# Performance work log

Measured on AMD Instinct MI355X. Metric: run time of the kernel, lower is better.

## Reference

```python
import jax, jax.numpy as jnp
import numpy as np

WS = 8      # window size
NH = 8      # num heads
ED = 256    # embed dim
HD = ED // NH  # head dim


def conv2d(x, w, b):
    # x: [B,C,H,W], w: [O,I,3,3] (torch OIHW), SAME padding, stride 1
    y = jax.lax.conv_general_dilated(x, w, (1, 1), 'SAME',
                                     dimension_numbers=('NCHW', 'OIHW', 'NCHW'))
    return y + b[None, :, None, None]


def linear(x, w, b):
    # torch Linear: y = x @ W^T + b, w: [out,in]
    return jnp.einsum('bnc,oc->bno', x, w) + b


def window_partition(x, ws):
    B, C, H, W = x.shape
    x = x.reshape(B, C, H // ws, ws, W // ws, ws)
    x = jnp.transpose(x, (0, 2, 4, 3, 5, 1))  # B, H/ws, W/ws, ws, ws, C
    return x.reshape(-1, ws * ws, C)


def window_reverse(win, H, W, ws, C):
    nW = (H // ws) * (W // ws)
    B = win.shape[0] // nW
    x = win.reshape(B, H // ws, W // ws, ws, ws, C)
    x = jnp.transpose(x, (0, 5, 1, 3, 2, 4))
    return x.reshape(B, C, H, W)


def setup_inputs() -> dict:
    key = jax.random.key(0)
    ks = jax.random.split(key, 24)
    s = 0.02
    inp = {
        'xmap': jax.random.normal(ks[0], (4, ED, 256, 256), jnp.float32),
        'xfeat': jax.random.normal(ks[1], (4, 32, 256, 256), jnp.float32),
        'cmap_w': jax.random.normal(ks[2], (ED, ED, 3, 3), jnp.float32) * s,
        'cmap_b': jnp.zeros((ED,), jnp.float32),
        'cfeat_w': jax.random.normal(ks[3], (ED, 32, 3, 3), jnp.float32) * s,
        'cfeat_b': jnp.zeros((ED,), jnp.float32),
        'qxmap_w': jax.random.normal(ks[4], (ED, ED), jnp.float32) * s,
        'qxmap_b': jnp.zeros((ED,), jnp.float32),
        'kxmap_w': jax.random.normal(ks[5], (ED, ED), jnp.float32) * s,
        'kxmap_b': jnp.zeros((ED,), jnp.float32),
        'vxmap_w': jax.random.normal(ks[6], (ED, ED), jnp.float32) * s,
        'vxmap_b': jnp.zeros((ED,), jnp.float32),
        'qxfeat_w': jax.random.normal(ks[7], (ED, ED), jnp.float32) * s,
        'qxfeat_b': jnp.zeros((ED,), jnp.float32),
        'kxfeat_w': jax.random.normal(ks[8], (ED, ED), jnp.float32) * s,
        'kxfeat_b': jnp.zeros((ED,), jnp.float32),
        'proj_w': jax.random.normal(ks[9], (ED, ED), jnp.float32) * s,
        'proj_b': jnp.zeros((ED,), jnp.float32),
        'cout_w': jax.random.normal(ks[10], (ED, ED, 3, 3), jnp.float32) * s,
        'cout_b': jnp.zeros((ED,), jnp.float32),
    }
    return inp


def reference(xmap, xfeat, cmap_w, cmap_b, cfeat_w, cfeat_b,
              qxmap_w, qxmap_b, kxmap_w, kxmap_b, vxmap_w, vxmap_b,
              qxfeat_w, qxfeat_b, kxfeat_w, kxfeat_b,
              proj_w, proj_b, cout_w, cout_b):
    B, C, H, W = xmap.shape  # xfeat matches spatial size -> no interpolate branch
    xmap = conv2d(xmap, cmap_w, cmap_b)
    identity = xmap
    wm = window_partition(xmap, WS)                        # [Bw, N, C]
    wf = window_partition(conv2d(xfeat, cfeat_w, cfeat_b), WS)
    Bw, N, _ = wm.shape

    def heads(t):
        return jnp.transpose(t.reshape(Bw, N, NH, HD), (0, 2, 1, 3))  # [Bw,H,N,D]

    q_m = heads(linear(wm, qxmap_w, qxmap_b))
    k_m = heads(linear(wm, kxmap_w, kxmap_b))
    v_m = heads(linear(wm, vxmap_w, vxmap_b))
    q_f = heads(linear(wf, qxfeat_w, qxfeat_b))
    k_f = heads(linear(wf, kxfeat_w, kxfeat_b))

    q_g = jax.nn.sigmoid(q_f) * q_m
    k_g = jax.nn.sigmoid(k_f) * k_m

    scale = 1.0 / jnp.sqrt(jnp.asarray(HD, q_g.dtype))
    attn = jax.nn.softmax(jnp.einsum('bhnd,bhmd->bhnm', q_g, k_g) * scale, axis=-1)
    out = jnp.einsum('bhnm,bhmd->bhnd', attn, v_m)         # [Bw,H,N,D]
    out = jnp.transpose(out, (0, 2, 1, 3)).reshape(Bw, N, C)
    out = window_reverse(linear(out, proj_w, proj_b), H, W, WS, C)
    return conv2d(out, cout_w, cout_b) + identity
```

## Files before the change

kernel.cpp:

```cpp
#include <hip/hip_runtime.h>
#include <hip/hip_bf16.h>
#include <cstdint>
#include <math.h>

using bf16 = __hip_bfloat16;
typedef __attribute__((ext_vector_type(4))) float f32x4;
typedef __attribute__((ext_vector_type(8))) short s16x8;
typedef __attribute__((ext_vector_type(4))) short s16x4;

#define AS3(p) ((__attribute__((address_space(3))) void *)(p))
#define AS1(p) ((const __attribute__((address_space(1))) void *)(p))

static constexpr int Himg = 256, Wimg = 256, Bimg = 4;
static constexpr int HWimg = Himg * Wimg;
static constexpr int Ttok = Bimg * HWimg;

__device__ __forceinline__ void gld16(bf16* lds, const bf16* g) {
  __builtin_amdgcn_global_load_lds(AS1(g), AS3(lds), 16, 0, 0);
}

__device__ __forceinline__ unsigned short f2u(float f) {
  bf16 b = __float2bfloat16(f);
  unsigned short u; __builtin_memcpy(&u, &b, 2); return u;
}

__device__ __forceinline__ int remap_lin(int bid, int total) {
  return (bid & 7) * (total >> 3) + (bid >> 3);
}
__device__ __forceinline__ void remap_tile(int bid, int total, int NY, int BMv, int& t0, int& n0) {
  int lin = remap_lin(bid, total);
  t0 = (lin / NY) * BMv;
  n0 = (lin % NY) * 128;
}

__global__ void k_zero4k(float* p) {
  p[blockIdx.x * 256 + threadIdx.x] = 0.f;
}

__global__ void k_castf2b(const float* __restrict__ s, bf16* __restrict__ d, int n) {
  int i = blockIdx.x * 256 + threadIdx.x;
  if (i < n) d[i] = __float2bfloat16(s[i]);
}

__global__ void k_copyf(const float* __restrict__ s, float* __restrict__ d, int n) {
  int i = blockIdx.x * 256 + threadIdx.x;
  if (i < n) d[i] = s[i];
}

__global__ void k_permconv(const float* __restrict__ w, bf16* __restrict__ o, int I) {
  int idx = blockIdx.x * 256 + threadIdx.x;
  int tot = 256 * 9 * I;
  if (idx >= tot) return;
  int i   = idx % I;
  int rem = idx / I;
  int tap = rem % 9;
  int oc  = rem / 9;
  o[idx] = __float2bfloat16(w[(oc * I + i) * 9 + tap]);
}

__global__ void k_tohwc(const float* __restrict__ src, bf16* __restrict__ dst, int C) {
  int bh = blockIdx.x;
  int w0 = blockIdx.y * 32;
  int c0 = blockIdx.z * 32;
  int b = bh / Himg, h = bh % Himg;
  __shared__ float tile[32][33];
  int tid = threadIdx.x;
  int x = tid & 31, y = tid >> 5;
  const float* sp = src + (size_t)b * C * HWimg + (size_t)h * Wimg;
#pragma unroll
  for (int p = 0; p < 4; ++p) {
    int cl = y + p * 8;
    tile[cl][x] = sp[(size_t)(c0 + cl) * HWimg + w0 + x];
  }
  __syncthreads();
#pragma unroll
  for (int p = 0; p < 4; ++p) {
    int wl = y + p * 8;
    dst[((size_t)bh * Wimg + w0 + wl) * C + c0 + x] = __float2bfloat16(tile[x][wl]);
  }
}

__global__ void k_tochw(const bf16* __restrict__ src, float* __restrict__ dst) {
  int bh = blockIdx.x, w0 = blockIdx.y * 32, c0 = blockIdx.z * 32;
  int b = bh >> 8, h = bh & 255;
  __shared__ float tile[32][33];
  int tid = threadIdx.x, x = tid & 31, y = tid >> 5;
  const bf16* sp = src + (size_t)bh * Wimg * 256;
#pragma unroll
  for (int p = 0; p < 4; ++p) {
    int wl = y + p * 8;
    tile[wl][x] = __bfloat162float(sp[(size_t)(w0 + wl) * 256 + c0 + x]);
  }
  __syncthreads();
#pragma unroll
  for (int p = 0; p < 4; ++p) {
    int cl = y + p * 8;
    dst[(((size_t)b * 256 + c0 + cl) * Himg + h) * Wimg + w0 + x] = tile[x][cl];
  }
}

template <int TAPS, int EPI>
__global__ void __launch_bounds__(512, 1)
k_gemm8(const bf16* __restrict__ Ain, const bf16* __restrict__ BT,
        const float* __restrict__ bias,
        bf16* __restrict__ outb, int ldo,
        const bf16* __restrict__ ident,
        const bf16* __restrict__ zp)
{
  constexpr int KTOT = TAPS * 256;
  const int t0 = remap_lin(blockIdx.x, gridDim.x) * 256;
  const int tid  = threadIdx.x;
  const int wave = tid >> 6, lane = tid & 63;
  const int wr = wave >> 2, wc = wave & 3;
  const int fr = lane & 15, fq = lane >> 4;

  __shared__ bf16 A0k0[256 * 32];
  __shared__ bf16 A0k1[256 * 32];
  __shared__ bf16 A1k0[256 * 32];
  __shared__ bf16 A1k1[256 * 32];
  __shared__ bf16 B0k0[256 * 32];
  __shared__ bf16 B0k1[256 * 32];
  __shared__ bf16 B1k0[256 * 32];
  __shared__ bf16 B1k1[256 * 32];

  f32x4 acc[8][4] = {};
  s16x8 bfr[4];

  const int slot8 = (fq ^ ((fr >> 1) & 3)) * 8;
  const int aoff  = (wr * 128 + fr) * 32 + slot8;
  const int boff  = (wc * 64 + fr) * 32 + slot8;
  const int ldsl  = (tid & 3) * 8;
  const int scol  = ((tid & 3) ^ ((tid >> 3) & 3)) * 8;
  const int srow  = tid >> 2;

  const bf16* Bb0 = BT + (size_t)srow * KTOT + scol;
  const bf16* Bb1 = BT + (size_t)(128 + srow) * KTOT + scol;
  const bf16* Aa0 = Ain + (size_t)(t0 + srow) * 256 + scol;
  const bf16* Aa1 = Ain + (size_t)(t0 + 128 + srow) * 256 + scol;
  const bf16 *a0c = Aa0, *a1c = Aa1, *a0n = Aa0, *a1n = Aa1;
  const int hU = (t0 >> 8) & 255;

  auto mkbase = [&](int tap, const bf16*& o0, const bf16*& o1) {
    const int dy = tap / 3 - 1, dx = tap % 3 - 1;
    const bool rowok = ((unsigned)(hU + dy)) < 256u;
    const long gb = (long)t0 + dy * Wimg + dx;
    o0 = (rowok && (unsigned)(srow + dx) < 256u)
             ? Ain + (gb + srow) * 256 + scol : zp + scol;
    o1 = (rowok && (unsigned)(128 + srow + dx) < 256u)
             ? Ain + (gb + 128 + srow) * 256 + scol : zp + scol;
  };

#define STA8(DST, P0, P1, CE) do {                                              \
    gld16(DST + srow * 32 + ldsl, (P0) + (CE));                                 \
    gld16(DST + (128 + srow) * 32 + ldsl, (P1) + (CE));                         \
  } while (0)
#define STB8(DST, KE) do {                                                      \
    gld16(DST + srow * 32 + ldsl, Bb0 + (KE));                                  \
    gld16(DST + (128 + srow) * 32 + ldsl, Bb1 + (KE));                          \
  } while (0)

#define NVMs
#define VM4 asm volatile("s_waitcnt vmcnt(4)" ::: "memory")
#define VM0 asm volatile("s_waitcnt vmcnt(0)" ::: "memory")

#define PHO(RA, RB, MH, READB, ...) do {                                         \
    s16x8 af_[4];                                                                \
    _Pragma("unroll") for (int q_ = 0; q_ < 4; ++q_)                             \
      af_[q_] = *(const s16x8*)((RA) + aoff + ((MH) * 4 + q_) * 512);            \
    if (READB) {                                                                 \
      _Pragma("unroll") for (int n_ = 0; n_ < 4; ++n_)                           \
        bfr[n_] = *(const s16x8*)((RB) + boff + n_ * 512);                       \
    }                                                                            \
    __VA_ARGS__;                                                                 \
    asm volatile("s_waitcnt lgkmcnt(0)" ::: "memory");                           \
    __builtin_amdgcn_sched_barrier(0);                                           \
    __builtin_amdgcn_s_setprio(1);                                               \
    _Pragma("unroll") for (int q_ = 0; q_ < 4; ++q_)                             \
      _Pragma("unroll") for (int n_ = 0; n_ < 4; ++n_)                           \
        acc[(MH) * 4 + q_][n_] = __builtin_amdgcn_mfma_f32_16x16x32_bf16(        \
            af_[q_], bfr[n_], acc[(MH) * 4 + q_][n_], 0, 0, 0);                  \
    __builtin_amdgcn_s_setprio(0);                                               \
  } while (0)

#define PHE(RA, RB, MH, READB, VMSTMT, ...) do {                                 \
    s16x8 af_[4];                                                                \
    _Pragma("unroll") for (int q_ = 0; q_ < 4; ++q_)                             \
      af_[q_] = *(const s16x8*)((RA) + aoff + ((MH) * 4 + q_) * 512);            \
    if (READB) {                                                                 \
      _Pragma("unroll") for (int n_ = 0; n_ < 4; ++n_)                           \
        bfr[n_] = *(const s16x8*)((RB) + boff + n_ * 512);                       \
    }                                                                            \
    __VA_ARGS__;                                                                 \
    VMSTMT;                                                                      \
    __builtin_amdgcn_sched_barrier(0);                                           \
    __builtin_amdgcn_s_barrier();                                                \
    asm volatile("s_waitcnt lgkmcnt(0)" ::: "memory");                           \
    __builtin_amdgcn_sched_barrier(0);                                           \
    __builtin_amdgcn_s_setprio(1);                                               \
    _Pragma("unroll") for (int q_ = 0; q_ < 4; ++q_)                             \
      _Pragma("unroll") for (int n_ = 0; n_ < 4; ++n_)                           \
        acc[(MH) * 4 + q_][n_] = __builtin_amdgcn_mfma_f32_16x16x32_bf16(        \
            af_[q_], bfr[n_], acc[(MH) * 4 + q_][n_], 0, 0, 0);                  \
    __builtin_amdgcn_s_setprio(0);                                               \
  } while (0)

  if constexpr (TAPS == 9) {
    mkbase(0, a0c, a1c);
    mkbase(1, a0n, a1n);
    STA8(A0k0, a0c, a1c, 0);  STB8(B0k0, 0);
    STA8(A0k1, a0c, a1c, 32); STB8(B0k1, 32);
    VM4;
    __builtin_amdgcn_s_barrier();
#pragma unroll 1
    for (int tap = 0; tap < 8; ++tap) {
      PHO(A0k0, B0k0, 0, 1, STA8(A1k0, a0c, a1c, 64));
      PHE(A0k0, B0k0, 1, 0, VM4, STB8(B1k0, 64));
      PHO(A0k1, B0k1, 0, 1, STA8(A1k1, a0c, a1c, 96));
      PHE(A0k1, B0k1, 1, 0, VM4, STB8(B1k1, 96));
      PHO(A1k0, B1k0, 0, 1, STA8(A0k0, a0c, a1c, 128));
      PHE(A1k0, B1k0, 1, 0, VM4, STB8(B0k0, 128));
      PHO(A1k1, B1k1, 0, 1, STA8(A0k1, a0c, a1c, 160));
      PHE(A1k1, B1k1, 1, 0, VM4, STB8(B0k1, 160));
      PHO(A0k0, B0k0, 0, 1, STA8(A1k0, a0c, a1c, 192));
      PHE(A0k0, B0k0, 1, 0, VM4, STB8(B1k0, 192));
      PHO(A0k1, B0k1, 0, 1, STA8(A1k1, a0c, a1c, 224));
      PHE(A0k1, B0k1, 1, 0, VM4, STB8(B1k1, 224));
      PHO(A1k0, B1k0, 0, 1, STA8(A0k0, a0n, a1n, 0));
      PHE(A1k0, B1k0, 1, 0, VM4, STB8(B0k0, 256));
      PHO(A1k1, B1k1, 0, 1, STA8(A0k1, a0n, a1n, 32));
      PHE(A1k1, B1k1, 1, 0, VM4, STB8(B0k1, 288));
      a0c = a0n; a1c = a1n;
      if (tap + 2 < 9) mkbase(tap + 2, a0n, a1n);
      Bb0 += 256; Bb1 += 256;
    }
    PHO(A0k0, B0k0, 0, 1, STA8(A1k0, a0c, a1c, 64));
    PHE(A0k0, B0k0, 1, 0, VM4, STB8(B1k0, 64));
    PHO(A0k1, B0k1, 0, 1, STA8(A1k1, a0c, a1c, 96));
    PHE(A0k1, B0k1, 1, 0, VM4, STB8(B1k1, 96));
    PHO(A1k0, B1k0, 0, 1, STA8(A0k0, a0c, a1c, 128));
    PHE(A1k0, B1k0, 1, 0, VM4, STB8(B0k0, 128));
    PHO(A1k1, B1k1, 0, 1, STA8(A0k1, a0c, a1c, 160));
    PHE(A1k1, B1k1, 1, 0, VM4, STB8(B0k1, 160));
    PHO(A0k0, B0k0, 0, 1, STA8(A1k0, a0c, a1c, 192));
    PHE(A0k0, B0k0, 1, 0, VM4, STB8(B1k0, 192));
    PHO(A0k1, B0k1, 0, 1, STA8(A1k1, a0c, a1c, 224));
    PHE(A0k1, B0k1, 1, 0, VM4, STB8(B1k1, 224));
    PHO(A1k0, B1k0, 0, 1, );
    PHE(A1k0, B1k0, 1, 0, VM0, );
    PHO(A1k1, B1k1, 0, 1, );
    PHE(A1k1, B1k1, 1, 0, NVMs, );
  } else {
    STA8(A0k0, Aa0, Aa1, 0);  STB8(B0k0, 0);
    STA8(A0k1, Aa0, Aa1, 32); STB8(B0k1, 32);
    VM4;
    __builtin_amdgcn_s_barrier();
    PHO(A0k0, B0k0, 0, 1, STA8(A1k0, Aa0, Aa1, 64));
    PHE(A0k0, B0k0, 1, 0, VM4, STB8(B1k0, 64));
    PHO(A0k1, B0k1, 0, 1, STA8(A1k1, Aa0, Aa1, 96));
    PHE(A0k1, B0k1, 1, 0, VM4, STB8(B1k1, 96));
    PHO(A1k0, B1k0, 0, 1, STA8(A0k0, Aa0, Aa1, 128));
    PHE(A1k0, B1k0, 1, 0, VM4, STB8(B0k0, 128));
    PHO(A1k1, B1k1, 0, 1, STA8(A0k1, Aa0, Aa1, 160));
    PHE(A1k1, B1k1, 1, 0, VM4, STB8(B0k1, 160));
    PHO(A0k0, B0k0, 0, 1, STA8(A1k0, Aa0, Aa1, 192));
    PHE(A0k0, B0k0, 1, 0, VM4, STB8(B1k0, 192));
    PHO(A0k1, B0k1, 0, 1, STA8(A1k1, Aa0, Aa1, 224));
    PHE(A0k1, B0k1, 1, 0, VM4, STB8(B1k1, 224));
    PHO(A1k0, B1k0, 0, 1, );
    PHE(A1k0, B1k0, 1, 0, VM0, );
    PHO(A1k1, B1k1, 0, 1, );
    PHE(A1k1, B1k1, 1, 0, NVMs, );
  }
#undef PHO
#undef PHE
#undef STA8
#undef STB8
#undef NVMs
#undef VM4
#undef VM0

#pragma unroll
  for (int m = 0; m < 8; ++m) {
#pragma unroll
    for (int n = 0; n < 4; ++n) {
      const int col = wc * 64 + n * 16 + fr;
#pragma unroll
      for (int j = 0; j < 4; ++j) {
        const int row = wr * 128 + m * 16 + fq * 4 + j;
        const size_t t = (size_t)t0 + row;
        float v = acc[m][n][j] + bias[col];
        if (EPI == 0) {
          outb[t * ldo + col] = __float2bfloat16(v);
        } else {
          v += __bfloat162float(ident[t * 256 + col]);
          outb[t * 256 + col] = __float2bfloat16(v);
        }
      }
    }
  }
}

template <int CIN, int TAPS, int EPI>
__global__ void __launch_bounds__(256, 2)
k_gemm(const bf16* __restrict__ Ain, const bf16* __restrict__ BT,
       const float* __restrict__ bias,
       bf16* __restrict__ outb, int ldo,
       const bf16* __restrict__ ident,
       const bf16* __restrict__ zp, int NY)
{
  constexpr int KTOT = TAPS * CIN;
  constexpr int NK = KTOT / 32;
  int t0, n0;
  remap_tile(blockIdx.x, gridDim.x, NY, 256, t0, n0);
  const int tid = threadIdx.x;
  const int wave = tid >> 6, lane = tid & 63;
  const int seg = lane & 3;
  const int rr  = lane >> 2;

  __shared__ bf16 sA0[256 * 32];
  __shared__ bf16 sA1[256 * 32];
  __shared__ bf16 sA2[256 * 32];
  __shared__ bf16 sB0[128 * 32];
  __shared__ bf16 sB1[128 * 32];
  __shared__ bf16 sB2[128 * 32];

  f32x4 acc[8][4] = {};

  const int wr = wave >> 1, wc = wave & 1;
  const int fr = lane & 15, fq = lane >> 4;
  const int sseg = (seg ^ ((rr >> 1) & 3)) * 8;
  const int slot = (fq ^ ((fr >> 1) & 3)) * 8;

#define STAGE(WA, WB, KSV) do {                                                 \
    const int k0_ = (KSV) * 32;                                                 \
    const int tap_ = k0_ / CIN;                                                 \
    const int c0_ = k0_ - tap_ * CIN;                                           \
    const int dy_ = tap_ / 3 - 1, dx_ = tap_ % 3 - 1;                           \
    _Pragma("unroll") for (int i_ = 0; i_ < 4; ++i_) {                          \
      const int g_ = i_ * 4 + wave;                                             \
      const int t_ = t0 + g_ * 16 + rr;                                         \
      const bf16* src_;                                                         \
      if (TAPS == 1) {                                                          \
        src_ = Ain + (size_t)t_ * CIN + k0_ + sseg;                             \
      } else {                                                                  \
        const int hh_ = ((t_ >> 8) & 255) + dy_, ww_ = (t_ & 255) + dx_;        \
        const bool v_ = ((unsigned)hh_ < 256u) && ((unsigned)ww_ < 256u);       \
        const long gi_ = (long)t_ + dy_ * Wimg + dx_;                           \
        src_ = v_ ? (Ain + gi_ * CIN + c0_ + sseg) : (zp + sseg);               \
      }                                                                         \
      gld16(WA + g_ * 16 * 32, src_);                                           \
    }                                                                           \
    _Pragma("unroll") for (int i_ = 0; i_ < 2; ++i_) {                          \
      const int g_ = i_ * 4 + wave;                                             \
      gld16(WB + g_ * 16 * 32,                                                  \
            BT + (size_t)(n0 + g_ * 16 + rr) * KTOT + k0_ + sseg);              \
    }                                                                           \
  } while (0)

#define GSTEP(RA, RB, WA, WB, KSV, LASTF) do {                                  \
    if (LASTF) { asm volatile("s_waitcnt vmcnt(0)" ::: "memory"); }             \
    else       { asm volatile("s_waitcnt vmcnt(6)" ::: "memory"); }             \
    __builtin_amdgcn_s_barrier();                                               \
    s16x8 af_[8], bf_[4];                                                       \
    _Pragma("unroll") for (int m_ = 0; m_ < 8; ++m_)                            \
      af_[m_] = *(const s16x8*)(RA + (wr * 128 + m_ * 16 + fr) * 32 + slot);    \
    _Pragma("unroll") for (int n_ = 0; n_ < 4; ++n_)                            \
      bf_[n_] = *(const s16x8*)(RB + (wc * 64 + n_ * 16 + fr) * 32 + slot);     \
    if ((KSV) + 2 < NK) STAGE(WA, WB, (KSV) + 2);                               \
    __builtin_amdgcn_s_setprio(1);                                              \
    _Pragma("unroll") for (int m_ = 0; m_ < 8; ++m_)                            \
      _Pragma("unroll") for (int n_ = 0; n_ < 4; ++n_)                          \
        acc[m_][n_] = __builtin_amdgcn_mfma_f32_16x16x32_bf16(af_[m_], bf_[n_], acc[m_][n_], 0, 0, 0); \
    __builtin_amdgcn_s_setprio(0);                                              \
  } while (0)

  STAGE(sA0, sB0, 0);
  STAGE(sA1, sB1, 1);

  constexpr int NMAIN = ((NK - 1) / 3) * 3;
  int ks = 0;
#pragma unroll 1
  for (; ks < NMAIN; ks += 3) {
    GSTEP(sA0, sB0, sA2, sB2, ks,     false);
    GSTEP(sA1, sB1, sA0, sB0, ks + 1, false);
    GSTEP(sA2, sB2, sA1, sB1, ks + 2, false);
  }
  constexpr int TREM = NK - NMAIN;
  if constexpr (TREM == 3) {
    GSTEP(sA0, sB0, sA2, sB2, NMAIN,     false);
    GSTEP(sA1, sB1, sA0, sB0, NMAIN + 1, false);
    GSTEP(sA2, sB2, sA1, sB1, NMAIN + 2, true);
  } else if constexpr (TREM == 2) {
    GSTEP(sA0, sB0, sA2, sB2, NMAIN,     false);
    GSTEP(sA1, sB1, sA0, sB0, NMAIN + 1, true);
  } else {
    GSTEP(sA0, sB0, sA2, sB2, NMAIN,     true);
  }
#undef GSTEP
#undef STAGE

#pragma unroll
  for (int m = 0; m < 8; ++m) {
#pragma unroll
    for (int n = 0; n < 4; ++n) {
      const int col = n0 + wc * 64 + n * 16 + fr;
#pragma unroll
      for (int j = 0; j < 4; ++j) {
        const int row = wr * 128 + m * 16 + fq * 4 + j;
        const size_t t = (size_t)t0 + row;
        float v = acc[m][n][j] + bias[col];
        if (EPI == 0) {
          outb[t * ldo + col] = __float2bfloat16(v);
        } else {
          v += __bfloat162float(ident[t * 256 + col]);
          outb[t * 256 + col] = __float2bfloat16(v);
        }
      }
    }
  }
}

__global__ void __launch_bounds__(256, 2)
k_gemm_qkv(const bf16* __restrict__ Am, const bf16* __restrict__ Af,
           const bf16* __restrict__ Bm, const bf16* __restrict__ Bf,
           const float* __restrict__ bm, const float* __restrict__ bfi,
           bf16* __restrict__ out)
{
  int t0, n0;
  remap_tile(blockIdx.x, gridDim.x, 4, 128, t0, n0);
  const int tid = threadIdx.x;
  const int wave = tid >> 6, lane = tid & 63;
  const int seg = lane & 3;
  const int rr  = lane >> 2;

  __shared__ bf16 sA0[128 * 32];
  __shared__ bf16 sA1[128 * 32];
  __shared__ bf16 sA2[128 * 32];
  __shared__ bf16 sB0[128 * 32];
  __shared__ bf16 sB1[128 * 32];
  __shared__ bf16 sB2[128 * 32];

  f32x4 accm[4][4] = {};
  f32x4 accf[4][4] = {};

  const int wr = wave >> 1, wc = wave & 1;
  const int fr = lane & 15, fq = lane >> 4;
  const int sseg = (seg ^ ((rr >> 1) & 3)) * 8;
  const int slot = (fq ^ ((fr >> 1) & 3)) * 8;

#define STAGEQ(WA, WB, SV) do {                                                 \
    const int k0_ = ((SV) >> 1) * 32;                                           \
    const bf16* A_ = ((SV) & 1) ? Af : Am;                                      \
    const bf16* B_ = ((SV) & 1) ? Bf : Bm;                                      \
    _Pragma("unroll") for (int i_ = 0; i_ < 2; ++i_) {                          \
      const int r_ = wave * 32 + i_ * 16 + rr;                                  \
      gld16(WA + (wave * 32 + i_ * 16) * 32, A_ + (size_t)(t0 + r_) * 256 + k0_ + sseg); \
      gld16(WB + (wave * 32 + i_ * 16) * 32, B_ + (size_t)(n0 + r_) * 256 + k0_ + sseg); \
    }                                                                           \
  } while (0)

#define QSTEP(RA, RB, WA, WB, SV, LASTF) do {                                   \
    if (LASTF) { asm volatile("s_waitcnt vmcnt(0)" ::: "memory"); }             \
    else       { asm volatile("s_waitcnt vmcnt(4)" ::: "memory"); }             \
    __builtin_amdgcn_s_barrier();                                               \
    s16x8 af_[4], bf_[4];                                                       \
    _Pragma("unroll") for (int m_ = 0; m_ < 4; ++m_)                            \
      af_[m_] = *(const s16x8*)(RA + (wr * 64 + m_ * 16 + fr) * 32 + slot);     \
    _Pragma("unroll") for (int n_ = 0; n_ < 4; ++n_)                            \
      bf_[n_] = *(const s16x8*)(RB + (wc * 64 + n_ * 16 + fr) * 32 + slot);     \
    if ((SV) + 2 < 16) STAGEQ(WA, WB, (SV) + 2);                                \
    __builtin_amdgcn_s_setprio(1);                                              \
    if ((SV) & 1) {                                                             \
      _Pragma("unroll") for (int m_ = 0; m_ < 4; ++m_)                          \
        _Pragma("unroll") for (int n_ = 0; n_ < 4; ++n_)                        \
          accf[m_][n_] = __builtin_amdgcn_mfma_f32_16x16x32_bf16(af_[m_], bf_[n_], accf[m_][n_], 0, 0, 0); \
    } else {                                                                    \
      _Pragma("unroll") for (int m_ = 0; m_ < 4; ++m_)                          \
        _Pragma("unroll") for (int n_ = 0; n_ < 4; ++n_)                        \
          accm[m_][n_] = __builtin_amdgcn_mfma_f32_16x16x32_bf16(af_[m_], bf_[n_], accm[m_][n_], 0, 0, 0); \
    }                                                                           \
    __builtin_amdgcn_s_setprio(0);                                              \
  } while (0)

  STAGEQ(sA0, sB0, 0);
  STAGEQ(sA1, sB1, 1);

  int s = 0;
#pragma unroll 1
  for (; s < 15; s += 3) {
    QSTEP(sA0, sB0, sA2, sB2, s,     false);
    QSTEP(sA1, sB1, sA0, sB0, s + 1, false);
    QSTEP(sA2, sB2, sA1, sB1, s + 2, false);
  }
  QSTEP(sA0, sB0, sA2, sB2, 15, true);
#undef QSTEP
#undef STAGEQ

#pragma unroll
  for (int m = 0; m < 4; ++m) {
#pragma unroll
    for (int n = 0; n < 4; ++n) {
      const int col = n0 + wc * 64 + n * 16 + fr;
#pragma unroll
      for (int j = 0; j < 4; ++j) {
        const int row = wr * 64 + m * 16 + fq * 4 + j;
        const size_t t = (size_t)t0 + row;
        float v = accm[m][n][j] + bm[col];
        const float g = accf[m][n][j] + bfi[col];
        v *= 1.f / (1.f + __expf(-g));
        out[t * 768 + col] = __float2bfloat16(v);
      }
    }
  }
}

__global__ void __launch_bounds__(256, 2)
k_attn_mfma(const bf16* __restrict__ qkv, bf16* __restrict__ out) {
  __shared__ short smem[4 * 7424];
  const int tid = threadIdx.x;
  const int wave = tid >> 6, lane = tid & 63;
  const int fr = lane & 15, fq = lane >> 4;
  const int wi = blockIdx.x >> 1;
  const int head = (blockIdx.x & 1) * 4 + wave;
  const int b = wi >> 10, rem = wi & 1023, wh = rem >> 5, ww = rem & 31;
  const size_t tbase = (size_t)b * HWimg + (size_t)(wh * 8) * Wimg + ww * 8;

  short* Qs = smem + wave * 7424;
  short* Ks = Qs + 2560;
  short* VT = Qs + 5120;
  short* P  = Qs;
  short* Ol = Qs;

  auto tok = [&](int i) -> size_t {
    return tbase + (size_t)(i >> 3) * Wimg + (i & 7);
  };

  {
    const bf16* tb = qkv + tok(lane) * 768 + head * 32;
#pragma unroll
    for (int c = 0; c < 4; ++c) {
      s16x8 qv = *(const s16x8*)(tb + c * 8);
      s16x8 kv = *(const s16x8*)(tb + 256 + c * 8);
      s16x8 vv = *(const s16x8*)(tb + 512 + c * 8);
      *(s16x8*)(Qs + lane * 40 + c * 8) = qv;
      *(s16x8*)(Ks + lane * 40 + c * 8) = kv;
#pragma unroll
      for (int e = 0; e < 8; ++e) VT[(c * 8 + e) * 72 + lane] = vv[e];
    }
  }

  s16x8 kf[4], qf[4];
#pragma unroll
  for (int m = 0; m < 4; ++m)
    kf[m] = *(const s16x8*)(Ks + (fr + 16 * m) * 40 + fq * 8);
#pragma unroll
  for (int n = 0; n < 4; ++n)
    qf[n] = *(const s16x8*)(Qs + (fr + 16 * n) * 40 + fq * 8);

  f32x4 st[4][4] = {};
#pragma unroll
  for (int m = 0; m < 4; ++m)
#pragma unroll
    for (int n = 0; n < 4; ++n)
      st[m][n] = __builtin_amdgcn_mfma_f32_16x16x32_bf16(kf[m], qf[n], st[m][n], 0, 0, 0);

  const float scale = 0.17677669529663688f;
  float invs[4];
#pragma unroll
  for (int n = 0; n < 4; ++n) {
    float mx = -1e30f;
#pragma unroll
    for (int m = 0; m < 4; ++m)
#pragma unroll
      for (int j = 0; j < 4; ++j) mx = fmaxf(mx, st[m][n][j]);
    mx = fmaxf(mx, __shfl_xor(mx, 16));
    mx = fmaxf(mx, __shfl_xor(mx, 32));
    float sum = 0.f;
#pragma unroll
    for (int m = 0; m < 4; ++m) {
      s16x4 pk;
#pragma unroll
      for (int j = 0; j < 4; ++j) {
        float e = __expf((st[m][n][j] - mx) * scale);
        sum += e;
        pk[j] = (short)f2u(e);
      }
      *(s16x4*)(P + (fr + 16 * n) * 72 + 16 * m + 4 * fq) = pk;
    }
    sum += __shfl_xor(sum, 16);
    sum += __shfl_xor(sum, 32);
    invs[n] = 1.f / sum;
  }

  f32x4 oc[4][2] = {};
#pragma unroll
  for (int ks = 0; ks < 2; ++ks) {
    s16x8 pf[4], vf[2];
#pragma unroll
    for (int m = 0; m < 4; ++m)
      pf[m] = *(const s16x8*)(P + (fr + 16 * m) * 72 + ks * 32 + fq * 8);
#pragma unroll
    for (int n = 0; n < 2; ++n)
      vf[n] = *(const s16x8*)(VT + (fr + 16 * n) * 72 + ks * 32 + fq * 8);
#pragma unroll
    for (int m = 0; m < 4; ++m)
#pragma unroll
      for (int n = 0; n < 2; ++n)
        oc[m][n] = __builtin_amdgcn_mfma_f32_16x16x32_bf16(pf[m], vf[n], oc[m][n], 0, 0, 0);
  }

#pragma unroll
  for (int m = 0; m < 4; ++m)
#pragma unroll
    for (int j = 0; j < 4; ++j) {
      const float inv = __shfl(invs[m], 4 * fq + j);
      const int q = 16 * m + 4 * fq + j;
#pragma unroll
      for (int n = 0; n < 2; ++n)
        Ol[q * 40 + fr + 16 * n] = (short)f2u(oc[m][n][j] * inv);
    }
  {
    bf16* op = out + tok(lane) * 256 + head * 32;
#pragma unroll
    for (int c = 0; c < 4; ++c)
      *(s16x8*)(op + c * 8) = *(const s16x8*)(Ol + lane * 40 + c * 8);
  }
}

extern "C" void kernel_launch(void* const* d_in, const int* in_sizes, int n_in,
                              void* d_out, int out_size, void* d_ws, size_t ws_size,
                              hipStream_t stream) {
  const float* xmap    = (const float*)d_in[0];
  const float* xfeat   = (const float*)d_in[1];
  const float* cmap_w  = (const float*)d_in[2];
  const float* cmap_b  = (const float*)d_in[3];
  const float* cfeat_w = (const float*)d_in[4];
  const float* cfeat_b = (const float*)d_in[5];
  const float* qxmap_w = (const float*)d_in[6];
  const float* qxmap_b = (const float*)d_in[7];
  const float* kxmap_w = (const float*)d_in[8];
  const float* kxmap_b = (const float*)d_in[9];
  const float* vxmap_w = (const float*)d_in[10];
  const float* vxmap_b = (const float*)d_in[11];
  const float* qxfeat_w = (const float*)d_in[12];
  const float* qxfeat_b = (const float*)d_in[13];
  const float* kxfeat_w = (const float*)d_in[14];
  const float* kxfeat_b = (const float*)d_in[15];
  const float* proj_w  = (const float*)d_in[16];
  const float* proj_b  = (const float*)d_in[17];
  const float* cout_w  = (const float*)d_in[18];
  const float* cout_b  = (const float*)d_in[19];

  uint8_t* ws = (uint8_t*)d_ws;
  size_t off = 0;
  auto alloc = [&](size_t bytes) -> void* {
    void* p = ws + off;
    off += (bytes + 255) & ~(size_t)255;
    return p;
  };
  float* zp       = (float*)alloc(4096);
  bf16* cmap_wT   = (bf16*)alloc((size_t)2304 * 256 * 2);
  bf16* cout_wT   = (bf16*)alloc((size_t)2304 * 256 * 2);
  bf16* cfeat_wT  = (bf16*)alloc((size_t)288 * 256 * 2);
  bf16* lin_qkv_wT= (bf16*)alloc((size_t)768 * 256 * 2);
  bf16* lin_f_wT  = (bf16*)alloc((size_t)512 * 256 * 2);
  bf16* proj_wT   = (bf16*)alloc((size_t)256 * 256 * 2);
  float* bias_qkv = (float*)alloc(768 * 4);
  float* bias_f   = (float*)alloc(512 * 4);
  bf16* xm_nhwc   = (bf16*)alloc((size_t)Ttok * 256 * 2);
  bf16* xf_nhwc   = (bf16*)alloc((size_t)Ttok * 32 * 2);
  bf16* xc        = (bf16*)alloc((size_t)Ttok * 256 * 2);
  bf16* fc        = (bf16*)alloc((size_t)Ttok * 256 * 2);
  bf16* qkv       = (bf16*)alloc((size_t)Ttok * 768 * 2);
  bf16* attn_out  = xm_nhwc;
  bf16* proj_out  = fc;
  bf16* convout   = qkv;
  bf16* zpb = (bf16*)zp;

  k_zero4k<<<4, 256, 0, stream>>>(zp);
  k_permconv<<<(256 * 9 * 256 + 255) / 256, 256, 0, stream>>>(cmap_w, cmap_wT, 256);
  k_permconv<<<(256 * 9 * 256 + 255) / 256, 256, 0, stream>>>(cout_w, cout_wT, 256);
  k_permconv<<<(256 * 9 * 32 + 255) / 256, 256, 0, stream>>>(cfeat_w, cfeat_wT, 32);
  k_castf2b<<<256, 256, 0, stream>>>(qxmap_w, lin_qkv_wT, 65536);
  k_castf2b<<<256, 256, 0, stream>>>(kxmap_w, lin_qkv_wT + 65536, 65536);
  k_castf2b<<<256, 256, 0, stream>>>(vxmap_w, lin_qkv_wT + 131072, 65536);
  k_castf2b<<<256, 256, 0, stream>>>(qxfeat_w, lin_f_wT, 65536);
  k_castf2b<<<256, 256, 0, stream>>>(kxfeat_w, lin_f_wT + 65536, 65536);
  k_castf2b<<<256, 256, 0, stream>>>(proj_w, proj_wT, 65536);
  k_copyf<<<1, 256, 0, stream>>>(qxmap_b, bias_qkv, 256);
  k_copyf<<<1, 256, 0, stream>>>(kxmap_b, bias_qkv + 256, 256);
  k_copyf<<<1, 256, 0, stream>>>(vxmap_b, bias_qkv + 512, 256);
  k_copyf<<<1, 256, 0, stream>>>(qxfeat_b, bias_f, 256);
  k_copyf<<<1, 256, 0, stream>>>(kxfeat_b, bias_f + 256, 256);

  k_tohwc<<<dim3(Bimg * Himg, Wimg / 32, 256 / 32), 256, 0, stream>>>(xmap, xm_nhwc, 256);
  k_tohwc<<<dim3(Bimg * Himg, Wimg / 32, 1), 256, 0, stream>>>(xfeat, xf_nhwc, 32);

  const int NB = Ttok / 256;
  k_gemm8<9, 0><<<dim3(NB), dim3(512), 0, stream>>>(
      xm_nhwc, cmap_wT, cmap_b, xc, 256, nullptr, zpb);
  k_gemm<32, 9, 0><<<dim3(NB * 2), dim3(256), 0, stream>>>(
      xf_nhwc, cfeat_wT, cfeat_b, fc, 256, nullptr, zpb, 2);
  k_gemm8<1, 0><<<dim3(NB), dim3(512), 0, stream>>>(
      xc, lin_qkv_wT + 131072, bias_qkv + 512, qkv + 512, 768, nullptr, zpb);
  k_gemm_qkv<<<dim3((Ttok / 128) * 4), dim3(256), 0, stream>>>(
      xc, fc, lin_qkv_wT, lin_f_wT, bias_qkv, bias_f, qkv);
  k_attn_mfma<<<dim3(4096 * 2), dim3(256), 0, stream>>>(qkv, attn_out);
  k_gemm8<1, 0><<<dim3(NB), dim3(512), 0, stream>>>(
      attn_out, proj_wT, proj_b, proj_out, 256, nullptr, zpb);
  k_gemm8<9, 2><<<dim3(NB), dim3(512), 0, stream>>>(
      proj_out, cout_wT, cout_b, convout, 256, xc, zpb);
  k_tochw<<<dim3(Bimg * Himg, Wimg / 32, 256 / 32), 256, 0, stream>>>(convout, (float*)d_out);
}
```

Before: 1.515 ms.

## Replace fused gated QK GEMM with two k_gemm8 passes using sigmoid and multiply epilogues

The dedicated k_gemm_qkv kernel, which computed the map and feature Q/K projections together and applied the sigmoid gate in registers, is removed. A first k_gemm8 pass writes sigmoid(feature projection) into the qkv buffer, and a second pass computes the map projection and multiplies it in place by the stored gate. k_gemm8 gains an N-tile parameter so it can cover 512 output columns with two column tiles. The aim is to reuse the faster 512-thread 256x256 GEMM instead of the smaller 128-tile kernel, at the cost of an extra write and read of the gate values through global memory.

```diff
diff --git a/kernel.cpp b/kernel.cpp
--- a/kernel.cpp
+++ b/kernel.cpp
@@ -105,10 +105,12 @@
         const float* __restrict__ bias,
         bf16* __restrict__ outb, int ldo,
         const bf16* __restrict__ ident,
-        const bf16* __restrict__ zp)
+        const bf16* __restrict__ zp, int NY)
 {
   constexpr int KTOT = TAPS * 256;
-  const int t0 = remap_lin(blockIdx.x, gridDim.x) * 256;
+  const int lin = remap_lin(blockIdx.x, gridDim.x);
+  const int t0 = (lin / NY) * 256;
+  const int n0 = (lin % NY) * 256;
   const int tid  = threadIdx.x;
   const int wave = tid >> 6, lane = tid & 63;
   const int wr = wave >> 2, wc = wave & 3;
@@ -133,8 +135,8 @@
   const int scol  = ((tid & 3) ^ ((tid >> 3) & 3)) * 8;
   const int srow  = tid >> 2;
 
-  const bf16* Bb0 = BT + (size_t)srow * KTOT + scol;
-  const bf16* Bb1 = BT + (size_t)(128 + srow) * KTOT + scol;
+  const bf16* Bb0 = BT + (size_t)(n0 + srow) * KTOT + scol;
+  const bf16* Bb1 = BT + (size_t)(n0 + 128 + srow) * KTOT + scol;
   const bf16* Aa0 = Ain + (size_t)(t0 + srow) * 256 + scol;
   const bf16* Aa1 = Ain + (size_t)(t0 + 128 + srow) * 256 + scol;
   const bf16 *a0c = Aa0, *a1c = Aa1, *a0n = Aa0, *a1n = Aa1;
@@ -283,7 +285,7 @@
   for (int m = 0; m < 8; ++m) {
 #pragma unroll
     for (int n = 0; n < 4; ++n) {
-      const int col = wc * 64 + n * 16 + fr;
+      const int col = n0 + wc * 64 + n * 16 + fr;
 #pragma unroll
       for (int j = 0; j < 4; ++j) {
         const int row = wr * 128 + m * 16 + fq * 4 + j;
@@ -291,9 +293,14 @@
         float v = acc[m][n][j] + bias[col];
         if (EPI == 0) {
           outb[t * ldo + col] = __float2bfloat16(v);
-        } else {
+        } else if (EPI == 1) {
+          outb[t * ldo + col] = __float2bfloat16(1.f / (1.f + __expf(-v)));
+        } else if (EPI == 2) {
           v += __bfloat162float(ident[t * 256 + col]);
           outb[t * 256 + col] = __float2bfloat16(v);
+        } else {
+          bf16* p = outb + t * ldo + col;
+          *p = __float2bfloat16(v * __bfloat162float(*p));
         }
       }
     }
@@ -421,100 +428,6 @@
 }
 
 __global__ void __launch_bounds__(256, 2)
-k_gemm_qkv(const bf16* __restrict__ Am, const bf16* __restrict__ Af,
-           const bf16* __restrict__ Bm, const bf16* __restrict__ Bf,
-           const float* __restrict__ bm, const float* __restrict__ bfi,
-           bf16* __restrict__ out)
-{
-  int t0, n0;
-  remap_tile(blockIdx.x, gridDim.x, 4, 128, t0, n0);
-  const int tid = threadIdx.x;
-  const int wave = tid >> 6, lane = tid & 63;
-  const int seg = lane & 3;
-  const int rr  = lane >> 2;
-
-  __shared__ bf16 sA0[128 * 32];
-  __shared__ bf16 sA1[128 * 32];
-  __shared__ bf16 sA2[128 * 32];
-  __shared__ bf16 sB0[128 * 32];
-  __shared__ bf16 sB1[128 * 32];
-  __shared__ bf16 sB2[128 * 32];
-
-  f32x4 accm[4][4] = {};
-  f32x4 accf[4][4] = {};
-
-  const int wr = wave >> 1, wc = wave & 1;
-  const int fr = lane & 15, fq = lane >> 4;
-  const int sseg = (seg ^ ((rr >> 1) & 3)) * 8;
-  const int slot = (fq ^ ((fr >> 1) & 3)) * 8;
-
-#define STAGEQ(WA, WB, SV) do {                                                 \
-    const int k0_ = ((SV) >> 1) * 32;                                           \
-    const bf16* A_ = ((SV) & 1) ? Af : Am;                                      \
-    const bf16* B_ = ((SV) & 1) ? Bf : Bm;                                      \
-    _Pragma("unroll") for (int i_ = 0; i_ < 2; ++i_) {                          \
-      const int r_ = wave * 32 + i_ * 16 + rr;                                  \
-      gld16(WA + (wave * 32 + i_ * 16) * 32, A_ + (size_t)(t0 + r_) * 256 + k0_ + sseg); \
-      gld16(WB + (wave * 32 + i_ * 16) * 32, B_ + (size_t)(n0 + r_) * 256 + k0_ + sseg); \
-    }                                                                           \
-  } while (0)
-
-#define QSTEP(RA, RB, WA, WB, SV, LASTF) do {                                   \
-    if (LASTF) { asm volatile("s_waitcnt vmcnt(0)" ::: "memory"); }             \
-    else       { asm volatile("s_waitcnt vmcnt(4)" ::: "memory"); }             \
-    __builtin_amdgcn_s_barrier();                                               \
-    s16x8 af_[4], bf_[4];                                                       \
-    _Pragma("unroll") for (int m_ = 0; m_ < 4; ++m_)                            \
-      af_[m_] = *(const s16x8*)(RA + (wr * 64 + m_ * 16 + fr) * 32 + slot);     \
-    _Pragma("unroll") for (int n_ = 0; n_ < 4; ++n_)                            \
-      bf_[n_] = *(const s16x8*)(RB + (wc * 64 + n_ * 16 + fr) * 32 + slot);     \
-    if ((SV) + 2 < 16) STAGEQ(WA, WB, (SV) + 2);                                \
-    __builtin_amdgcn_s_setprio(1);                                              \
-    if ((SV) & 1) {                                                             \
-      _Pragma("unroll") for (int m_ = 0; m_ < 4; ++m_)                          \
-        _Pragma("unroll") for (int n_ = 0; n_ < 4; ++n_)                        \
-          accf[m_][n_] = __builtin_amdgcn_mfma_f32_16x16x32_bf16(af_[m_], bf_[n_], accf[m_][n_], 0, 0, 0); \
-    } else {                                                                    \
-      _Pragma("unroll") for (int m_ = 0; m_ < 4; ++m_)                          \
-        _Pragma("unroll") for (int n_ = 0; n_ < 4; ++n_)                        \
-          accm[m_][n_] = __builtin_amdgcn_mfma_f32_16x16x32_bf16(af_[m_], bf_[n_], accm[m_][n_], 0, 0, 0); \
-    }                                                                           \
-    __builtin_amdgcn_s_setprio(0);                                              \
-  } while (0)
-
-  STAGEQ(sA0, sB0, 0);
-  STAGEQ(sA1, sB1, 1);
-
-  int s = 0;
-#pragma unroll 1
-  for (; s < 15; s += 3) {
-    QSTEP(sA0, sB0, sA2, sB2, s,     false);
-    QSTEP(sA1, sB1, sA0, sB0, s + 1, false);
-    QSTEP(sA2, sB2, sA1, sB1, s + 2, false);
-  }
-  QSTEP(sA0, sB0, sA2, sB2, 15, true);
-#undef QSTEP
-#undef STAGEQ
-
-#pragma unroll
-  for (int m = 0; m < 4; ++m) {
-#pragma unroll
-    for (int n = 0; n < 4; ++n) {
-      const int col = n0 + wc * 64 + n * 16 + fr;
-#pragma unroll
-      for (int j = 0; j < 4; ++j) {
-        const int row = wr * 64 + m * 16 + fq * 4 + j;
-        const size_t t = (size_t)t0 + row;
-        float v = accm[m][n][j] + bm[col];
-        const float g = accf[m][n][j] + bfi[col];
-        v *= 1.f / (1.f + __expf(-g));
-        out[t * 768 + col] = __float2bfloat16(v);
-      }
-    }
-  }
-}
-
-__global__ void __launch_bounds__(256, 2)
 k_attn_mfma(const bf16* __restrict__ qkv, bf16* __restrict__ out) {
   __shared__ short smem[4 * 7424];
   const int tid = threadIdx.x;
@@ -698,17 +611,19 @@
 
   const int NB = Ttok / 256;
   k_gemm8<9, 0><<<dim3(NB), dim3(512), 0, stream>>>(
-      xm_nhwc, cmap_wT, cmap_b, xc, 256, nullptr, zpb);
+      xm_nhwc, cmap_wT, cmap_b, xc, 256, nullptr, zpb, 1);
   k_gemm<32, 9, 0><<<dim3(NB * 2), dim3(256), 0, stream>>>(
       xf_nhwc, cfeat_wT, cfeat_b, fc, 256, nullptr, zpb, 2);
+  k_gemm8<1, 1><<<dim3(NB * 2), dim3(512), 0, stream>>>(
+      fc, lin_f_wT, bias_f, qkv, 768, nullptr, zpb, 2);
   k_gemm8<1, 0><<<dim3(NB), dim3(512), 0, stream>>>(
-      xc, lin_qkv_wT + 131072, bias_qkv + 512, qkv + 512, 768, nullptr, zpb);
-  k_gemm_qkv<<<dim3((Ttok / 128) * 4), dim3(256), 0, stream>>>(
-      xc, fc, lin_qkv_wT, lin_f_wT, bias_qkv, bias_f, qkv);
+      xc, lin_qkv_wT + 131072, bias_qkv + 512, qkv + 512, 768, nullptr, zpb, 1);
+  k_gemm8<1, 3><<<dim3(NB * 2), dim3(512), 0, stream>>>(
+      xc, lin_qkv_wT, bias_qkv, qkv, 768, nullptr, zpb, 2);
   k_attn_mfma<<<dim3(4096 * 2), dim3(256), 0, stream>>>(qkv, attn_out);
   k_gemm8<1, 0><<<dim3(NB), dim3(512), 0, stream>>>(
-      attn_out, proj_wT, proj_b, proj_out, 256, nullptr, zpb);
+      attn_out, proj_wT, proj_b, proj_out, 256, nullptr, zpb, 1);
   k_gemm8<9, 2><<<dim3(NB), dim3(512), 0, stream>>>(
-      proj_out, cout_wT, cout_b, convout, 256, xc, zpb);
+      proj_out, cout_wT, cout_b, convout, 256, xc, zpb, 1);
   k_tochw<<<dim3(Bimg * Himg, Wimg / 32, 256 / 32), 256, 0, stream>>>(convout, (float*)d_out);
 }
```

Result: slower. 1.801 ms (+18.8%).

## Fuse NHWC-to-NCHW fp32 transpose into final conv GEMM epilogue

Applied to the files above, without the earlier changes.

The final 3x3 conv GEMM now adds bias and the residual, transposes its 256x256 output tile through a shared-memory arena, and writes fp32 NCHW directly to the output. This removes the separate k_tochw kernel along with the bf16 round-trip through an intermediate buffer. In exchange, shared memory is enlarged to about 130KB for all gemm8 instances and the epilogue gains two barrier-separated chunk passes.

```diff
diff --git a/kernel.cpp b/kernel.cpp
--- a/kernel.cpp
+++ b/kernel.cpp
@@ -80,30 +80,11 @@
   }
 }
 
-__global__ void k_tochw(const bf16* __restrict__ src, float* __restrict__ dst) {
-  int bh = blockIdx.x, w0 = blockIdx.y * 32, c0 = blockIdx.z * 32;
-  int b = bh >> 8, h = bh & 255;
-  __shared__ float tile[32][33];
-  int tid = threadIdx.x, x = tid & 31, y = tid >> 5;
-  const bf16* sp = src + (size_t)bh * Wimg * 256;
-#pragma unroll
-  for (int p = 0; p < 4; ++p) {
-    int wl = y + p * 8;
-    tile[wl][x] = __bfloat162float(sp[(size_t)(w0 + wl) * 256 + c0 + x]);
-  }
-  __syncthreads();
-#pragma unroll
-  for (int p = 0; p < 4; ++p) {
-    int cl = y + p * 8;
-    dst[(((size_t)b * 256 + c0 + cl) * Himg + h) * Wimg + w0 + x] = tile[x][cl];
-  }
-}
-
 template <int TAPS, int EPI>
 __global__ void __launch_bounds__(512, 1)
 k_gemm8(const bf16* __restrict__ Ain, const bf16* __restrict__ BT,
         const float* __restrict__ bias,
-        bf16* __restrict__ outb, int ldo,
+        bf16* __restrict__ outb, int ldo, float* __restrict__ outf,
         const bf16* __restrict__ ident,
         const bf16* __restrict__ zp)
 {
@@ -114,14 +95,15 @@
   const int wr = wave >> 2, wc = wave & 3;
   const int fr = lane & 15, fq = lane >> 4;
 
-  __shared__ bf16 A0k0[256 * 32];
-  __shared__ bf16 A0k1[256 * 32];
-  __shared__ bf16 A1k0[256 * 32];
-  __shared__ bf16 A1k1[256 * 32];
-  __shared__ bf16 B0k0[256 * 32];
-  __shared__ bf16 B0k1[256 * 32];
-  __shared__ bf16 B1k0[256 * 32];
-  __shared__ bf16 B1k1[256 * 32];
+  __shared__ __attribute__((aligned(16))) char arena[132608];
+  bf16* A0k0 = (bf16*)(arena);
+  bf16* A0k1 = (bf16*)(arena + 16384);
+  bf16* A1k0 = (bf16*)(arena + 32768);
+  bf16* A1k1 = (bf16*)(arena + 49152);
+  bf16* B0k0 = (bf16*)(arena + 65536);
+  bf16* B0k1 = (bf16*)(arena + 81920);
+  bf16* B1k0 = (bf16*)(arena + 98304);
+  bf16* B1k1 = (bf16*)(arena + 114688);
 
   f32x4 acc[8][4] = {};
   s16x8 bfr[4];
@@ -279,6 +261,42 @@
 #undef VM4
 #undef VM0
 
+  if (EPI == 2) {
+    float* TR = (float*)arena;
+    const int bN = t0 >> 16, hN = (t0 >> 8) & 255;
+#pragma unroll 1
+    for (int chunk = 0; chunk < 2; ++chunk) {
+      __builtin_amdgcn_s_barrier();
+      if ((wc >> 1) == chunk) {
+#pragma unroll
+        for (int m = 0; m < 8; ++m)
+#pragma unroll
+          for (int n = 0; n < 4; ++n) {
+            const int col = wc * 64 + n * 16 + fr;
+            const int cl  = (wc & 1) * 64 + n * 16 + fr;
+            const float bb = bias[col];
+#pragma unroll
+            for (int j = 0; j < 4; ++j) {
+              const int row = wr * 128 + m * 16 + fq * 4 + j;
+              const size_t t = (size_t)t0 + row;
+              TR[cl * 259 + row] = acc[m][n][j] + bb +
+                                   __bfloat162float(ident[t * 256 + col]);
+            }
+          }
+      }
+      __builtin_amdgcn_s_barrier();
+      {
+        const int cl = tid >> 2, wo = (tid & 3) * 4;
+        const int c = chunk * 128 + cl;
+        float* dp = outf + (((size_t)bN * 256 + c) * 256 + hN) * 256;
+#pragma unroll
+        for (int q = 0; q < 16; ++q)
+          *(f32x4*)(dp + wo + q * 16) = *(const f32x4*)&TR[cl * 259 + wo + q * 16];
+      }
+    }
+    return;
+  }
+
 #pragma unroll
   for (int m = 0; m < 8; ++m) {
 #pragma unroll
@@ -288,13 +306,7 @@
       for (int j = 0; j < 4; ++j) {
         const int row = wr * 128 + m * 16 + fq * 4 + j;
         const size_t t = (size_t)t0 + row;
-        float v = acc[m][n][j] + bias[col];
-        if (EPI == 0) {
-          outb[t * ldo + col] = __float2bfloat16(v);
-        } else {
-          v += __bfloat162float(ident[t * 256 + col]);
-          outb[t * 256 + col] = __float2bfloat16(v);
-        }
+        outb[t * ldo + col] = __float2bfloat16(acc[m][n][j] + bias[col]);
       }
     }
   }
@@ -674,7 +686,6 @@
   bf16* qkv       = (bf16*)alloc((size_t)Ttok * 768 * 2);
   bf16* attn_out  = xm_nhwc;
   bf16* proj_out  = fc;
-  bf16* convout   = qkv;
   bf16* zpb = (bf16*)zp;
 
   k_zero4k<<<4, 256, 0, stream>>>(zp);
@@ -698,17 +709,16 @@
 
   const int NB = Ttok / 256;
   k_gemm8<9, 0><<<dim3(NB), dim3(512), 0, stream>>>(
-      xm_nhwc, cmap_wT, cmap_b, xc, 256, nullptr, zpb);
+      xm_nhwc, cmap_wT, cmap_b, xc, 256, nullptr, nullptr, zpb);
   k_gemm<32, 9, 0><<<dim3(NB * 2), dim3(256), 0, stream>>>(
       xf_nhwc, cfeat_wT, cfeat_b, fc, 256, nullptr, zpb, 2);
   k_gemm8<1, 0><<<dim3(NB), dim3(512), 0, stream>>>(
-      xc, lin_qkv_wT + 131072, bias_qkv + 512, qkv + 512, 768, nullptr, zpb);
+      xc, lin_qkv_wT + 131072, bias_qkv + 512, qkv + 512, 768, nullptr, nullptr, zpb);
   k_gemm_qkv<<<dim3((Ttok / 128) * 4), dim3(256), 0, stream>>>(
       xc, fc, lin_qkv_wT, lin_f_wT, bias_qkv, bias_f, qkv);
   k_attn_mfma<<<dim3(4096 * 2), dim3(256), 0, stream>>>(qkv, attn_out);
   k_gemm8<1, 0><<<dim3(NB), dim3(512), 0, stream>>>(
-      attn_out, proj_wT, proj_b, proj_out, 256, nullptr, zpb);
+      attn_out, proj_wT, proj_b, proj_out, 256, nullptr, nullptr, zpb);
   k_gemm8<9, 2><<<dim3(NB), dim3(512), 0, stream>>>(
-      proj_out, cout_wT, cout_b, convout, 256, xc, zpb);
-  k_tochw<<<dim3(Bimg * Himg, Wimg / 32, 256 / 32), 256, 0, stream>>>(convout, (float*)d_out);
-}
+      proj_out, cout_wT, cout_b, nullptr, 0, (float*)d_out, xc, zpb);
+}
```

Result: faster. 1.396 ms (-7.9%).
